# Kernel tuning notes

Measured on AMD Instinct MI355X. Metric: run time of the kernel, lower is better.

Reference implementation:

```python
import jax, jax.numpy as jnp
import numpy as np

N = 8192          # nodes
F_IN = 256        # input_channel
F_OUT = 256       # output_channel
AVG_DEG = 32


def setup_inputs() -> dict:
    key = jax.random.key(0)
    k_a, k_x, k_w = jax.random.split(key, 3)
    # Dense 0/1 adjacency with avg degree ~AVG_DEG, plus self-loops so every
    # row has at least one neighbor (original code errors on isolated nodes).
    A = (jax.random.uniform(k_a, (N, N)) < (AVG_DEG / N)).astype(jnp.float32)
    A = jnp.maximum(A, jnp.eye(N, dtype=jnp.float32))
    deg = jnp.sum(A, axis=1)              # [N], >= 1
    D = jnp.diag(deg)                     # [N,N] diagonal degree matrix
    X = jax.random.normal(k_x, (N, F_IN), dtype=jnp.float32)
    W = jax.random.normal(k_w, (F_OUT, F_IN), dtype=jnp.float32) * (1.0 / np.sqrt(F_IN))
    b = jnp.zeros((F_OUT,), dtype=jnp.float32)
    return {"D": D, "X": X, "A": A, "W": W, "b": b}


def reference(D, X, A, W, b):
    # Vectorized form of the per-node python loop:
    #   for node i: neighbors j where A[i,j]!=0,
    #     dj = deg of each neighbor (row-max of D), dj0 = deg of FIRST neighbor
    #     coeff_j = 1/sqrt(dj0 * dj_j); agg_i = sum_j coeff_j * X[j]
    #     out_i = leaky_relu(agg_i @ W.T + b)
    degvec = jnp.max(D, axis=1)                       # [N] node degrees
    mask = A > 0                                      # [N,N] neighbor mask
    first_idx = jnp.argmax(mask, axis=1)              # first (lowest-index) neighbor of each node
    dj0 = degvec[first_idx]                           # [N]
    coeff = jnp.where(mask,
                      1.0 / jnp.sqrt(dj0[:, None] * degvec[None, :]),
                      0.0)                            # [N,N] normalized weights
    agg = coeff @ X                                   # [N,F_IN] weighted neighbor sum
    out = jax.nn.leaky_relu(agg @ W.T + b, negative_slope=0.01)  # [N,F_OUT]
    return out
```

## Files before the change

kernel.cpp:

```cpp
#include <hip/hip_runtime.h>
#include <hip/hip_bf16.h>

#define N_NODES 8192
#define F 256
#define CAP 512

typedef __attribute__((ext_vector_type(8))) short bf16x8;
typedef __attribute__((ext_vector_type(4))) float f32x4;

__device__ inline short f2bf_bits(float f) {
    __hip_bfloat16 h = __float2bfloat16(f);
    return *reinterpret_cast<short*>(&h);
}

__device__ inline bf16x8 load_cvt8(const float* __restrict__ p) {
    float4 v0 = *reinterpret_cast<const float4*>(p);
    float4 v1 = *reinterpret_cast<const float4*>(p + 4);
    bf16x8 r;
    r[0] = f2bf_bits(v0.x); r[1] = f2bf_bits(v0.y);
    r[2] = f2bf_bits(v0.z); r[3] = f2bf_bits(v0.w);
    r[4] = f2bf_bits(v1.x); r[5] = f2bf_bits(v1.y);
    r[6] = f2bf_bits(v1.z); r[7] = f2bf_bits(v1.w);
    return r;
}

__global__ __launch_bounds__(256) void k_rsd(const float* __restrict__ D,
                                             float* __restrict__ rsd) {
    int i = blockIdx.x * blockDim.x + threadIdx.x;
    if (i < N_NODES) rsd[i] = rsqrtf(D[(size_t)i * (N_NODES + 1)]);
}

__global__ __launch_bounds__(256) void k_gemm_z(const float* __restrict__ X,
                                                const float* __restrict__ W,
                                                const float* __restrict__ rsd,
                                                __hip_bfloat16* __restrict__ Zb) {
    const int tid  = threadIdx.x;
    const int lane = tid & 63;
    const int w    = tid >> 6;
    const int wr   = w >> 1, wc = w & 1;
    const int rb   = blockIdx.x * 128 + wr * 64;
    const int cb   = blockIdx.y * 64  + wc * 32;
    const int lrow = lane & 15;
    const int lk8  = (lane >> 4) * 8;

    f32x4 acc[4][2] = {};
    #pragma unroll
    for (int ks = 0; ks < 8; ++ks) {
        const int k0 = ks * 32 + lk8;
        bf16x8 a[4], b[2];
        #pragma unroll
        for (int m = 0; m < 4; ++m)
            a[m] = load_cvt8(X + (size_t)(rb + m * 16 + lrow) * F + k0);
        #pragma unroll
        for (int n = 0; n < 2; ++n)
            b[n] = load_cvt8(W + (size_t)(cb + n * 16 + lrow) * F + k0);
        #pragma unroll
        for (int m = 0; m < 4; ++m)
            #pragma unroll
            for (int n = 0; n < 2; ++n)
                acc[m][n] = __builtin_amdgcn_mfma_f32_16x16x32_bf16(a[m], b[n], acc[m][n], 0, 0, 0);
    }
    const int crow0 = (lane >> 4) * 4;
    const int ccol  = lane & 15;
    #pragma unroll
    for (int m = 0; m < 4; ++m) {
        #pragma unroll
        for (int r = 0; r < 4; ++r) {
            const int row = rb + m * 16 + crow0 + r;
            const float s = rsd[row];
            #pragma unroll
            for (int n = 0; n < 2; ++n) {
                const int col = cb + n * 16 + ccol;
                Zb[(size_t)row * F + col] = __float2bfloat16(acc[m][n][r] * s);
            }
        }
    }
}

__global__ __launch_bounds__(256) void k_scan_gather(const float* __restrict__ A,
                                                     const __hip_bfloat16* __restrict__ Zb,
                                                     const float* __restrict__ rsd,
                                                     const float* __restrict__ bias,
                                                     float* __restrict__ out) {
    __shared__ int s_cnt;
    __shared__ int s_min;
    __shared__ int s_list[CAP];

    const int tid = threadIdx.x;
    const int row = blockIdx.x;
    if (tid == 0) { s_cnt = 0; s_min = N_NODES; }
    __syncthreads();

    const float4* Arow = reinterpret_cast<const float4*>(A + (size_t)row * N_NODES);
    int localmin = N_NODES;
    #pragma unroll
    for (int kk = 0; kk < 8; ++kk) {
        const float4 v = Arow[kk * 256 + tid];
        const int c0 = (kk * 256 + tid) * 4;
        if (v.x != 0.f) { int p = atomicAdd(&s_cnt, 1); if (p < CAP) s_list[p] = c0;     if (c0     < localmin) localmin = c0;     }
        if (v.y != 0.f) { int p = atomicAdd(&s_cnt, 1); if (p < CAP) s_list[p] = c0 + 1; if (c0 + 1 < localmin) localmin = c0 + 1; }
        if (v.z != 0.f) { int p = atomicAdd(&s_cnt, 1); if (p < CAP) s_list[p] = c0 + 2; if (c0 + 2 < localmin) localmin = c0 + 2; }
        if (v.w != 0.f) { int p = atomicAdd(&s_cnt, 1); if (p < CAP) s_list[p] = c0 + 3; if (c0 + 3 < localmin) localmin = c0 + 3; }
    }
    if (localmin < N_NODES) atomicMin(&s_min, localmin);
    __syncthreads();

    const int n = min(s_cnt, CAP);
    const float scale = rsd[s_min];

    float acc = 0.f;
    for (int t = 0; t < n; ++t) {
        const int j = s_list[t];
        acc += __bfloat162float(Zb[(size_t)j * F + tid]);
    }
    const float y = scale * acc + bias[tid];
    out[(size_t)row * F + tid] = (y > 0.f) ? y : 0.01f * y;
}

extern "C" void kernel_launch(void* const* d_in, const int* in_sizes, int n_in,
                              void* d_out, int out_size, void* d_ws, size_t ws_size,
                              hipStream_t stream) {
    const float* D = (const float*)d_in[0];
    const float* X = (const float*)d_in[1];
    const float* A = (const float*)d_in[2];
    const float* W = (const float*)d_in[3];
    const float* b = (const float*)d_in[4];
    float* out = (float*)d_out;

    float* rsd = (float*)d_ws;
    __hip_bfloat16* Zb = (__hip_bfloat16*)((char*)d_ws + N_NODES * sizeof(float));

    k_rsd<<<N_NODES / 256, 256, 0, stream>>>(D, rsd);
    k_gemm_z<<<dim3(N_NODES / 128, F / 64), 256, 0, stream>>>(X, W, rsd, Zb);
    k_scan_gather<<<N_NODES, 256, 0, stream>>>(A, Zb, rsd, b, out);
}
```

Baseline: 498.5 us.

## Fuse rsqrt-degree into GEMM, shrink GEMM tile, nontemporal A loads, unroll gather

Drops the separate rsd kernel. The GEMM now computes rsqrt of the diagonal of D into shared memory per block, and the gather kernel reads D directly for the first-neighbour scale. The GEMM tile shrinks from 128 to 64 rows so more blocks are launched. The A scan uses nontemporal loads, the neighbour gather is unrolled by 8 to raise memory-level parallelism, and the output is written with nontemporal stores. This saves a launch and intermediate traffic but adds an extra strided D read per gather block.

```diff
diff --git a/kernel.cpp b/kernel.cpp
--- a/kernel.cpp
+++ b/kernel.cpp
@@ -24,54 +24,56 @@
     return r;
 }
 
-__global__ __launch_bounds__(256) void k_rsd(const float* __restrict__ D,
-                                             float* __restrict__ rsd) {
-    int i = blockIdx.x * blockDim.x + threadIdx.x;
-    if (i < N_NODES) rsd[i] = rsqrtf(D[(size_t)i * (N_NODES + 1)]);
-}
-
 __global__ __launch_bounds__(256) void k_gemm_z(const float* __restrict__ X,
                                                 const float* __restrict__ W,
-                                                const float* __restrict__ rsd,
+                                                const float* __restrict__ D,
                                                 __hip_bfloat16* __restrict__ Zb) {
+    __shared__ float s_rsd[64];
     const int tid  = threadIdx.x;
+    const int bx   = blockIdx.x, by = blockIdx.y;
+    if (tid < 64)
+        s_rsd[tid] = rsqrtf(D[(size_t)(bx * 64 + tid) * (N_NODES + 1)]);
+
     const int lane = tid & 63;
     const int w    = tid >> 6;
     const int wr   = w >> 1, wc = w & 1;
-    const int rb   = blockIdx.x * 128 + wr * 64;
-    const int cb   = blockIdx.y * 64  + wc * 32;
+    const int rb   = bx * 64 + wr * 32;
+    const int cb   = by * 64 + wc * 32;
     const int lrow = lane & 15;
     const int lk8  = (lane >> 4) * 8;
 
-    f32x4 acc[4][2] = {};
+    f32x4 acc[2][2] = {};
     #pragma unroll
     for (int ks = 0; ks < 8; ++ks) {
         const int k0 = ks * 32 + lk8;
-        bf16x8 a[4], b[2];
+        bf16x8 a[2], b[2];
         #pragma unroll
-        for (int m = 0; m < 4; ++m)
+        for (int m = 0; m < 2; ++m)
             a[m] = load_cvt8(X + (size_t)(rb + m * 16 + lrow) * F + k0);
         #pragma unroll
         for (int n = 0; n < 2; ++n)
             b[n] = load_cvt8(W + (size_t)(cb + n * 16 + lrow) * F + k0);
         #pragma unroll
-        for (int m = 0; m < 4; ++m)
+        for (int m = 0; m < 2; ++m)
             #pragma unroll
             for (int n = 0; n < 2; ++n)
                 acc[m][n] = __builtin_amdgcn_mfma_f32_16x16x32_bf16(a[m], b[n], acc[m][n], 0, 0, 0);
     }
+    __syncthreads();
+
     const int crow0 = (lane >> 4) * 4;
     const int ccol  = lane & 15;
     #pragma unroll
-    for (int m = 0; m < 4; ++m) {
+    for (int m = 0; m < 2; ++m) {
         #pragma unroll
         for (int r = 0; r < 4; ++r) {
-            const int row = rb + m * 16 + crow0 + r;
-            const float s = rsd[row];
+            const int lrowi = wr * 32 + m * 16 + crow0 + r;
+            const float s = s_rsd[lrowi];
+            const size_t row = (size_t)bx * 64 + lrowi;
             #pragma unroll
             for (int n = 0; n < 2; ++n) {
                 const int col = cb + n * 16 + ccol;
-                Zb[(size_t)row * F + col] = __float2bfloat16(acc[m][n][r] * s);
+                Zb[row * F + col] = __float2bfloat16(acc[m][n][r] * s);
             }
         }
     }
@@ -79,7 +81,7 @@
 
 __global__ __launch_bounds__(256) void k_scan_gather(const float* __restrict__ A,
                                                      const __hip_bfloat16* __restrict__ Zb,
-                                                     const float* __restrict__ rsd,
+                                                     const float* __restrict__ D,
                                                      const float* __restrict__ bias,
                                                      float* __restrict__ out) {
     __shared__ int s_cnt;
@@ -91,30 +93,45 @@
     if (tid == 0) { s_cnt = 0; s_min = N_NODES; }
     __syncthreads();
 
-    const float4* Arow = reinterpret_cast<const float4*>(A + (size_t)row * N_NODES);
+    const f32x4* Arow = reinterpret_cast<const f32x4*>(A + (size_t)row * N_NODES);
     int localmin = N_NODES;
     #pragma unroll
     for (int kk = 0; kk < 8; ++kk) {
-        const float4 v = Arow[kk * 256 + tid];
+        const f32x4 v = __builtin_nontemporal_load(&Arow[kk * 256 + tid]);
         const int c0 = (kk * 256 + tid) * 4;
-        if (v.x != 0.f) { int p = atomicAdd(&s_cnt, 1); if (p < CAP) s_list[p] = c0;     if (c0     < localmin) localmin = c0;     }
-        if (v.y != 0.f) { int p = atomicAdd(&s_cnt, 1); if (p < CAP) s_list[p] = c0 + 1; if (c0 + 1 < localmin) localmin = c0 + 1; }
-        if (v.z != 0.f) { int p = atomicAdd(&s_cnt, 1); if (p < CAP) s_list[p] = c0 + 2; if (c0 + 2 < localmin) localmin = c0 + 2; }
-        if (v.w != 0.f) { int p = atomicAdd(&s_cnt, 1); if (p < CAP) s_list[p] = c0 + 3; if (c0 + 3 < localmin) localmin = c0 + 3; }
+        #pragma unroll
+        for (int e = 0; e < 4; ++e) {
+            if (v[e] != 0.f) {
+                int p = atomicAdd(&s_cnt, 1);
+                if (p < CAP) s_list[p] = c0 + e;
+                if (c0 + e < localmin) localmin = c0 + e;
+            }
+        }
     }
     if (localmin < N_NODES) atomicMin(&s_min, localmin);
     __syncthreads();
 
     const int n = min(s_cnt, CAP);
-    const float scale = rsd[s_min];
+    const float scale = rsqrtf(D[(size_t)s_min * (N_NODES + 1)]);
 
     float acc = 0.f;
-    for (int t = 0; t < n; ++t) {
-        const int j = s_list[t];
-        acc += __bfloat162float(Zb[(size_t)j * F + tid]);
+    int t = 0;
+    for (; t + 8 <= n; t += 8) {
+        int   j[8];
+        float v[8];
+        #pragma unroll
+        for (int u = 0; u < 8; ++u) j[u] = s_list[t + u];
+        #pragma unroll
+        for (int u = 0; u < 8; ++u) v[u] = __bfloat162float(Zb[(size_t)j[u] * F + tid]);
+        #pragma unroll
+        for (int u = 0; u < 8; ++u) acc += v[u];
     }
+    for (; t < n; ++t)
+        acc += __bfloat162float(Zb[(size_t)s_list[t] * F + tid]);
+
     const float y = scale * acc + bias[tid];
-    out[(size_t)row * F + tid] = (y > 0.f) ? y : 0.01f * y;
+    const float r = (y > 0.f) ? y : 0.01f * y;
+    __builtin_nontemporal_store(r, &out[(size_t)row * F + tid]);
 }
 
 extern "C" void kernel_launch(void* const* d_in, const int* in_sizes, int n_in,
@@ -127,10 +144,8 @@
     const float* b = (const float*)d_in[4];
     float* out = (float*)d_out;
 
-    float* rsd = (float*)d_ws;
-    __hip_bfloat16* Zb = (__hip_bfloat16*)((char*)d_ws + N_NODES * sizeof(float));
+    __hip_bfloat16* Zb = (__hip_bfloat16*)d_ws;
 
-    k_rsd<<<N_NODES / 256, 256, 0, stream>>>(D, rsd);
-    k_gemm_z<<<dim3(N_NODES / 128, F / 64), 256, 0, stream>>>(X, W, rsd, Zb);
-    k_scan_gather<<<N_NODES, 256, 0, stream>>>(A, Zb, rsd, b, out);
+    k_gemm_z<<<dim3(N_NODES / 64, F / 64), 256, 0, stream>>>(X, W, D, Zb);
+    k_scan_gather<<<N_NODES, 256, 0, stream>>>(A, Zb, D, b, out);
 }
```

Result: faster. 474.4 us (-4.8%).
